# Performance work log

Measured on AMD Instinct MI355X. Metric: run time of the kernel, lower is better.

Reference implementation:

```python
import jax, jax.numpy as jnp
import numpy as np


def setup_inputs() -> dict:
    key = jax.random.key(0)
    k1, k2 = jax.random.split(key)
    B, T, D = 32, 512, 384
    MAX_LEN = 3584  # >= T * (max_duration-1) so no utterance is truncated
    x = jax.random.normal(k1, (B, T, D), dtype=jnp.float32)
    duration = jax.random.randint(k2, (B, T), 0, 8, dtype=jnp.int32)
    return {"x": x, "duration": duration, "max_len": MAX_LEN}


def reference(x, duration, max_len):
    """Length regulator: repeat each phoneme vector x[b, t] duration[b, t]
    times along time, pad each utterance to max_len with zeros.
    Vectorized via cumulative-duration offsets + searchsorted gather
    (replaces the per-frame Python expand/cat loop of the original).
    Returns (output [B, max_len, D], mel_len [B]).
    """
    B, T, D = x.shape
    cum = jnp.cumsum(duration, axis=1)            # [B, T] exclusive-right boundaries
    mel_len = cum[:, -1].astype(jnp.int64)        # [B]
    positions = jnp.arange(max_len)               # [M]
    # frame m of utterance b comes from phoneme index = first t with cum[b,t] > m
    idx = jax.vmap(lambda c: jnp.searchsorted(c, positions, side="right"))(cum)  # [B, M]
    idx = jnp.clip(idx, 0, T - 1)
    valid = positions[None, :] < mel_len[:, None]  # [B, M] padding mask
    out = jnp.take_along_axis(x, idx[:, :, None], axis=1)  # [B, M, D]
    out = out * valid[:, :, None].astype(x.dtype)
    return out, mel_len
```

## Files before the change

kernel.cpp:

```cpp
#include <hip/hip_runtime.h>


#define LR_B 32
#define LR_T 512

__global__ void lr_scan_idx_kernel(const int* __restrict__ dur,
                                   int* __restrict__ idx,
                                   float* __restrict__ mel_out,
                                   int T, int max_len) {
    __shared__ int s[LR_T];
    const int b = blockIdx.x;
    const int t = threadIdx.x;
    s[t] = dur[b * T + t];
    __syncthreads();
    #pragma unroll
    for (int off = 1; off < LR_T; off <<= 1) {
        int add = (t >= off) ? s[t - off] : 0;
        __syncthreads();
        s[t] += add;
        __syncthreads();
    }
    const int total = s[T - 1];
    if (t == 0) {
        mel_out[b] = (float)total;
    }
    int* __restrict__ idxb = idx + b * max_len;
    for (int m = t; m < max_len; m += LR_T) {
        int r = -1;
        if (m < total) {
            int lo = 0, hi = T;
            while (lo < hi) {
                int mid = (lo + hi) >> 1;
                if (s[mid] <= m) lo = mid + 1; else hi = mid;
            }
            r = (lo < T) ? lo : (T - 1);
        }
        idxb[m] = r;
    }
}

template <int D4C>
__global__ void lr_copy_kernel(const float4* __restrict__ x4,
                               const int* __restrict__ idx,
                               float4* __restrict__ out4,
                               int T, int max_len) {
    const int b = blockIdx.y;
    const int tot = max_len * D4C;
    const int base = blockIdx.x * 1024 + threadIdx.x;
    const int* __restrict__ idxb = idx + b * max_len;
    const float4* __restrict__ xb = x4 + (size_t)b * T * D4C;
    float4* __restrict__ ob = out4 + (size_t)b * tot;
    #pragma unroll
    for (int j = 0; j < 4; ++j) {
        const int e  = base + j * 256;
        const int m  = e / D4C;
        const int d4 = e - m * D4C;
        const int id = idxb[m];
        float4 v = make_float4(0.f, 0.f, 0.f, 0.f);
        if (id >= 0) v = xb[id * D4C + d4];
        ob[e] = v;
    }
}

__global__ void lr_copy_generic(const float4* __restrict__ x4,
                                const int* __restrict__ idx,
                                float4* __restrict__ out4,
                                int T, int max_len, int D4) {
    const int b = blockIdx.y;
    const int tot = max_len * D4;
    const int e = blockIdx.x * blockDim.x + threadIdx.x;
    if (e >= tot) return;
    const int m  = e / D4;
    const int d4 = e - m * D4;
    const int id = idx[b * max_len + m];
    float4 v = make_float4(0.f, 0.f, 0.f, 0.f);
    if (id >= 0) v = x4[((size_t)b * T + id) * D4 + d4];
    out4[(size_t)b * tot + e] = v;
}

extern "C" void kernel_launch(void* const* d_in, const int* in_sizes, int n_in,
                              void* d_out, int out_size, void* d_ws, size_t ws_size,
                              hipStream_t stream) {
    const float* x   = (const float*)d_in[0];
    const int*   dur = (const int*)d_in[1];

    const int B = LR_B;
    const int T = LR_T;
    const int D = in_sizes[0] / in_sizes[1];
    const int max_len = (out_size / B - 1) / D;
    const int D4 = D / 4;

    float* out     = (float*)d_out;
    float* mel_out = out + (size_t)B * max_len * D;

    int* idx = (int*)d_ws;

    lr_scan_idx_kernel<<<B, T, 0, stream>>>(dur, idx, mel_out, T, max_len);

    const int tot = max_len * D4;
    if (D4 == 96 && (tot % 1024) == 0) {
        dim3 grid(tot / 1024, B, 1);
        lr_copy_kernel<96><<<grid, dim3(256, 1, 1), 0, stream>>>(
            (const float4*)x, idx, (float4*)d_out, T, max_len);
    } else {
        dim3 grid((tot + 255) / 256, B, 1);
        lr_copy_generic<<<grid, dim3(256, 1, 1), 0, stream>>>(
            (const float4*)x, idx, (float4*)d_out, T, max_len, D4);
    }
}
```

Measured before the change: 37.99 us.

## Fuse duration scan and index search into the gather-copy kernel

Replaces the separate scan/index kernel and copy kernel with one fused kernel. Each block recomputes the prefix sum of durations in shared memory, then binary-searches only the frame indices it needs into shared memory. This removes a kernel launch and the global idx write/read. Output stores become nontemporal. The cost is redundant scan work in every block.

Measured after the change: 35.15 us. 1.08x faster.

```diff
diff --git a/kernel.cpp b/kernel.cpp
--- a/kernel.cpp
+++ b/kernel.cpp
@@ -3,6 +3,75 @@
 
 #define LR_B 32
 #define LR_T 512
+
+typedef float f32x4 __attribute__((ext_vector_type(4)));
+
+template <int D4C>
+__global__ __launch_bounds__(256) void lr_fused_kernel(
+        const f32x4* __restrict__ x4,
+        const int* __restrict__ dur,
+        f32x4* __restrict__ out4,
+        float* __restrict__ mel_out,
+        int T, int max_len) {
+    __shared__ int s[LR_T];
+    __shared__ int idx_s[16];
+
+    const int b  = blockIdx.y;
+    const int bx = blockIdx.x;
+    const int t  = threadIdx.x;
+
+    const int* __restrict__ db = dur + b * LR_T;
+    s[t]       = db[t];
+    s[t + 256] = db[t + 256];
+    __syncthreads();
+    #pragma unroll
+    for (int off = 1; off < LR_T; off <<= 1) {
+        const int p1 = t + 256;
+        const int a0 = (t >= off) ? s[t - off] : 0;
+        const int a1 = s[p1 - off];
+        __syncthreads();
+        s[t]  += a0;
+        s[p1] += a1;
+        __syncthreads();
+    }
+    const int total = s[LR_T - 1];
+
+    if (bx == 0 && t == 0) {
+        mel_out[b] = (float)total;
+    }
+
+    const int e0 = bx * 1024;
+    const int m0 = e0 / D4C;
+    const int m1 = (e0 + 1023) / D4C;
+    const int NF = m1 - m0 + 1;
+    if (t < NF) {
+        const int m = m0 + t;
+        int r = -1;
+        if (m < total) {
+            int lo = 0, hi = T;
+            while (lo < hi) {
+                const int mid = (lo + hi) >> 1;
+                if (s[mid] <= m) lo = mid + 1; else hi = mid;
+            }
+            r = (lo < T) ? lo : (T - 1);
+        }
+        idx_s[t] = r;
+    }
+    __syncthreads();
+
+    const f32x4* __restrict__ xb = x4 + (size_t)b * T * D4C;
+    f32x4* __restrict__ ob = out4 + (size_t)b * (size_t)max_len * D4C;
+    #pragma unroll
+    for (int j = 0; j < 4; ++j) {
+        const int e  = e0 + j * 256 + t;
+        const int m  = e / D4C;
+        const int d4 = e - m * D4C;
+        const int id = idx_s[m - m0];
+        f32x4 v = (f32x4){0.f, 0.f, 0.f, 0.f};
+        if (id >= 0) v = xb[id * D4C + d4];
+        __builtin_nontemporal_store(v, &ob[e]);
+    }
+}
 
 __global__ void lr_scan_idx_kernel(const int* __restrict__ dur,
                                    int* __restrict__ idx,
@@ -21,9 +90,7 @@
         __syncthreads();
     }
     const int total = s[T - 1];
-    if (t == 0) {
-        mel_out[b] = (float)total;
-    }
+    if (t == 0) mel_out[b] = (float)total;
     int* __restrict__ idxb = idx + b * max_len;
     for (int m = t; m < max_len; m += LR_T) {
         int r = -1;
@@ -39,32 +106,9 @@
     }
 }
 
-template <int D4C>
-__global__ void lr_copy_kernel(const float4* __restrict__ x4,
-                               const int* __restrict__ idx,
-                               float4* __restrict__ out4,
-                               int T, int max_len) {
-    const int b = blockIdx.y;
-    const int tot = max_len * D4C;
-    const int base = blockIdx.x * 1024 + threadIdx.x;
-    const int* __restrict__ idxb = idx + b * max_len;
-    const float4* __restrict__ xb = x4 + (size_t)b * T * D4C;
-    float4* __restrict__ ob = out4 + (size_t)b * tot;
-    #pragma unroll
-    for (int j = 0; j < 4; ++j) {
-        const int e  = base + j * 256;
-        const int m  = e / D4C;
-        const int d4 = e - m * D4C;
-        const int id = idxb[m];
-        float4 v = make_float4(0.f, 0.f, 0.f, 0.f);
-        if (id >= 0) v = xb[id * D4C + d4];
-        ob[e] = v;
-    }
-}
-
-__global__ void lr_copy_generic(const float4* __restrict__ x4,
+__global__ void lr_copy_generic(const f32x4* __restrict__ x4,
                                 const int* __restrict__ idx,
-                                float4* __restrict__ out4,
+                                f32x4* __restrict__ out4,
                                 int T, int max_len, int D4) {
     const int b = blockIdx.y;
     const int tot = max_len * D4;
@@ -73,7 +117,7 @@
     const int m  = e / D4;
     const int d4 = e - m * D4;
     const int id = idx[b * max_len + m];
-    float4 v = make_float4(0.f, 0.f, 0.f, 0.f);
+    f32x4 v = (f32x4){0.f, 0.f, 0.f, 0.f};
     if (id >= 0) v = x4[((size_t)b * T + id) * D4 + d4];
     out4[(size_t)b * tot + e] = v;
 }
@@ -85,26 +129,24 @@
     const int*   dur = (const int*)d_in[1];
 
     const int B = LR_B;
-    const int T = LR_T;
+    const int T = in_sizes[1] / B;
     const int D = in_sizes[0] / in_sizes[1];
     const int max_len = (out_size / B - 1) / D;
     const int D4 = D / 4;
+    const int tot = max_len * D4;
 
     float* out     = (float*)d_out;
     float* mel_out = out + (size_t)B * max_len * D;
 
-    int* idx = (int*)d_ws;
-
-    lr_scan_idx_kernel<<<B, T, 0, stream>>>(dur, idx, mel_out, T, max_len);
-
-    const int tot = max_len * D4;
-    if (D4 == 96 && (tot % 1024) == 0) {
+    if (T == LR_T && D4 == 96 && (tot % 1024) == 0) {
         dim3 grid(tot / 1024, B, 1);
-        lr_copy_kernel<96><<<grid, dim3(256, 1, 1), 0, stream>>>(
-            (const float4*)x, idx, (float4*)d_out, T, max_len);
+        lr_fused_kernel<96><<<grid, dim3(256, 1, 1), 0, stream>>>(
+            (const f32x4*)x, dur, (f32x4*)d_out, mel_out, T, max_len);
     } else {
+        int* idx = (int*)d_ws;
+        lr_scan_idx_kernel<<<B, T, 0, stream>>>(dur, idx, mel_out, T, max_len);
         dim3 grid((tot + 255) / 256, B, 1);
         lr_copy_generic<<<grid, dim3(256, 1, 1), 0, stream>>>(
-            (const float4*)x, idx, (float4*)d_out, T, max_len, D4);
+            (const f32x4*)x, idx, (f32x4*)d_out, T, max_len, D4);
     }
 }
```
